# Performance work log

Measured on AMD Instinct MI355X. Metric: run time of the kernel, lower is better.

Reference implementation:

```python
import jax, jax.numpy as jnp
import numpy as np

N, M, D_IN, D_OUT = 100000, 1024, 64, 64


def setup_inputs() -> dict:
    key = jax.random.key(0)
    ks = jax.random.split(key, 8)
    # kaiming_uniform_ bound for fan_in = D_IN: sqrt(6 / fan_in) with a=sqrt(5) default? torch's
    # kaiming_uniform_ default (a=0) gives bound = sqrt(6/fan_in); exact init is irrelevant for math.
    bound = float(np.sqrt(6.0 / D_IN))
    return {
        "x": jax.random.normal(ks[0], (N, D_IN), dtype=jnp.float32),
        "neighbors": jax.random.normal(ks[1], (M, D_IN), dtype=jnp.float32),
        "Wq": jax.random.uniform(ks[2], (D_OUT, D_IN), jnp.float32, -bound, bound),
        "bq": jnp.zeros((D_OUT,), jnp.float32),
        "Wk": jax.random.uniform(ks[3], (D_OUT, D_IN), jnp.float32, -bound, bound),
        "bk": jnp.zeros((D_OUT,), jnp.float32),
        "Wv": jax.random.uniform(ks[4], (D_OUT, D_IN), jnp.float32, -bound, bound),
        "bv": jnp.zeros((D_OUT,), jnp.float32),
    }


def reference(x, neighbors, Wq, bq, Wk, bk, Wv, bv):
    # q: [N, D_OUT], k: [M, D_OUT]
    q = x @ Wq.T + bq
    k = neighbors @ Wk.T + bk
    # scores: [N, M] -- same math as sum(q[:,None,:] * k[None,:,:], axis=2) but via GEMM
    scores = q @ k.T
    attn = jax.nn.softmax(scores, axis=1)
    # attn @ neighbors: [N, D_IN], then value projection -> [N, D_OUT]
    agg = attn @ neighbors
    return agg @ Wv.T + bv
```

## Files before the change

kernel.cpp:

```cpp
#include <hip/hip_runtime.h>


#define N_ROWS 100000

typedef __attribute__((ext_vector_type(8))) _Float16 half8;
typedef __attribute__((ext_vector_type(4))) float    f32x4;

#define MFMA16(a,b,c) __builtin_amdgcn_mfma_f32_16x16x32_f16((a),(b),(c),0,0,0)

static __device__ __forceinline__ f32x4 zero4() {
    f32x4 v = {0.f, 0.f, 0.f, 0.f};
    return v;
}

__global__ __launch_bounds__(256)
void prep_kernel(const float* __restrict__ nb, const float* __restrict__ Wq,
                 const float* __restrict__ bq, const float* __restrict__ Wk,
                 unsigned short* __restrict__ GFh, unsigned short* __restrict__ GFl,
                 float* __restrict__ uW, unsigned short* __restrict__ KF,
                 unsigned short* __restrict__ VF)
{
    __shared__ __align__(16) float sm[8192];
    const int tid = threadIdx.x;
    if (blockIdx.x == 0) {
        const float4* wk4 = (const float4*)Wk;
        const float4* wq4 = (const float4*)Wq;
        float4* dk = (float4*)sm;
        float4* dq = (float4*)(sm + 4096);
        #pragma unroll
        for (int u = 0; u < 4; u++) {
            dk[u * 256 + tid] = wk4[u * 256 + tid];
            dq[u * 256 + tid] = wq4[u * 256 + tid];
        }
        __syncthreads();
        const int e2 = tid & 63, e1g = (tid >> 6) * 16;
        float g[16];
        #pragma unroll
        for (int q = 0; q < 16; q++) g[q] = 0.f;
        for (int w = 0; w < 64; w++) {
            float kv = sm[w * 64 + e2];
            const float* wqp = sm + 4096 + w * 64 + e1g;
            #pragma unroll
            for (int q = 0; q < 16; q++) g[q] = fmaf(wqp[q], kv, g[q]);
        }
        union { half8 h; uint4 u; } ph0, pl0, ph1, pl1;
        #pragma unroll
        for (int i = 0; i < 8; i++) {
            _Float16 h0 = (_Float16)g[i];
            ph0.h[i] = h0; pl0.h[i] = (_Float16)(g[i] - (float)h0);
            _Float16 h1 = (_Float16)g[8 + i];
            ph1.h[i] = h1; pl1.h[i] = (_Float16)(g[8 + i] - (float)h1);
        }
        const int mt = e2 >> 4, cc = e2 & 15;
        const int ks = tid >> 7, Q0 = 2 * ((tid >> 6) & 1);
        const int f  = mt * 2 + ks;
        *(uint4*)(GFh + (f * 64 + Q0 * 16 + cc) * 8)       = ph0.u;
        *(uint4*)(GFh + (f * 64 + (Q0 + 1) * 16 + cc) * 8) = ph1.u;
        *(uint4*)(GFl + (f * 64 + Q0 * 16 + cc) * 8)       = pl0.u;
        *(uint4*)(GFl + (f * 64 + (Q0 + 1) * 16 + cc) * 8) = pl1.u;
        if (tid < 64) {
            float uu = 0.f;
            for (int w = 0; w < 64; w++) uu = fmaf(bq[w], sm[w * 64 + tid], uu);
            uW[tid] = uu;
        }
    } else {
        const int j0 = (blockIdx.x - 1) * 64;
        const int T0 = (blockIdx.x - 1) * 2;
        {
            const int jr = tid >> 2, c0 = (tid & 3) * 16;
            const float* np = nb + (size_t)(j0 + jr) * 64 + c0;
            #pragma unroll
            for (int u = 0; u < 4; u++) {
                float4 v = *(const float4*)(np + 4 * u);
                sm[jr * 65 + c0 + 4 * u]     = v.x;
                sm[jr * 65 + c0 + 4 * u + 1] = v.y;
                sm[jr * 65 + c0 + 4 * u + 2] = v.z;
                sm[jr * 65 + c0 + 4 * u + 3] = v.w;
            }
        }
        #pragma unroll
        for (int s = 0; s < 2; s++) {
            const int slot = tid + 256 * s;
            const int tt = (slot >> 8) & 1, f = (slot >> 6) & 3, ln = slot & 63;
            const int t = f >> 1, h = f & 1, Qw = ln >> 4, cw = ln & 15;
            const int key = ((cw >> 3) & 1) * 16 + ((cw >> 2) & 1) * 8 + 4 * t + (cw & 3);
            const float* kp = nb + (size_t)((T0 + tt) * 32 + key) * 64 + h * 32 + Qw * 8;
            float b[8];
            *(float4*)b       = *(const float4*)kp;
            *(float4*)(b + 4) = *(const float4*)(kp + 4);
            union { half8 hh; uint4 u; } pk;
            #pragma unroll
            for (int i = 0; i < 8; i++) pk.hh[i] = (_Float16)b[i];
            *(uint4*)(KF + (size_t)(T0 + tt) * 2048 + f * 512 + ln * 8) = pk.u;
        }
        __syncthreads();
        #pragma unroll
        for (int s = 0; s < 2; s++) {
            const int slot = tid + 256 * s;
            const int tt = (slot >> 8) & 1, dt = (slot >> 6) & 3, ln = slot & 63;
            const int Qw = ln >> 4, cw = ln & 15;
            union { half8 hh; uint4 u; } pv;
            #pragma unroll
            for (int i = 0; i < 8; i++)
                pv.hh[i] = (_Float16)sm[(tt * 32 + Qw * 8 + i) * 65 + dt * 16 + cw];
            *(uint4*)(VF + (size_t)(T0 + tt) * 2048 + dt * 512 + ln * 8) = pv.u;
        }
    }
}

static __device__ __forceinline__ void flash_step(
    const unsigned short* __restrict__ kfl, const unsigned short* __restrict__ vfl,
    int Tn,
    const half8 (&ck)[4], half8 (&nk)[4], half8 (&vA)[4],
    const half8 (&qh)[2][2], const half8 (&ql)[2][2],
    f32x4 (&acc)[2][4], float (&mrow)[2], float (&lrow)[2])
{
    const unsigned short* kn = kfl + Tn * 2048;
    #pragma unroll
    for (int f = 0; f < 4; f++) nk[f] = *(const half8*)(kn + f * 512);

    f32x4 S[2][2];
    #pragma unroll
    for (int t = 0; t < 2; t++)
        #pragma unroll
        for (int qt = 0; qt < 2; qt++) {
            f32x4 s = MFMA16(ck[2 * t],     qh[qt][0], zero4());
            s = MFMA16(ck[2 * t + 1], qh[qt][1], s);
            s = MFMA16(ck[2 * t],     ql[qt][0], s);
            s = MFMA16(ck[2 * t + 1], ql[qt][1], s);
            S[t][qt] = s;
        }
    half8 pB[2];
    #pragma unroll
    for (int qt = 0; qt < 2; qt++) {
        float pmax = fmaxf(fmaxf(fmaxf(S[0][qt][0], S[0][qt][1]),
                                 fmaxf(S[0][qt][2], S[0][qt][3])),
                           fmaxf(fmaxf(S[1][qt][0], S[1][qt][1]),
                                 fmaxf(S[1][qt][2], S[1][qt][3])));
        if (__any(pmax > mrow[qt] + 8.f)) {
            float cm = pmax;
            cm = fmaxf(cm, __shfl_xor(cm, 16));
            cm = fmaxf(cm, __shfl_xor(cm, 32));
            const float mn = fmaxf(mrow[qt], cm);
            const float sc = __expf(mrow[qt] - mn);
            mrow[qt] = mn;
            lrow[qt] *= sc;
            #pragma unroll
            for (int dt = 0; dt < 4; dt++)
                #pragma unroll
                for (int r = 0; r < 4; r++) acc[qt][dt][r] *= sc;
        }
        const float mref = mrow[qt];
        float p[8]; float ps = 0.f;
        #pragma unroll
        for (int r = 0; r < 4; r++) { p[r] = __expf(S[0][qt][r] - mref); ps += p[r]; }
        #pragma unroll
        for (int r = 0; r < 4; r++) { p[4 + r] = __expf(S[1][qt][r] - mref); ps += p[4 + r]; }
        lrow[qt] += ps;
        #pragma unroll
        for (int i = 0; i < 8; i++) pB[qt][i] = (_Float16)p[i];
    }
    #pragma unroll
    for (int dt = 0; dt < 4; dt++) {
        acc[0][dt] = MFMA16(vA[dt], pB[0], acc[0][dt]);
        acc[1][dt] = MFMA16(vA[dt], pB[1], acc[1][dt]);
    }
    const unsigned short* vn = vfl + Tn * 2048;
    #pragma unroll
    for (int d = 0; d < 4; d++) vA[d] = *(const half8*)(vn + d * 512);
}

__global__ __launch_bounds__(64, 3)
void attn_kernel(const float* __restrict__ x,
                 const unsigned short* __restrict__ GFh,
                 const unsigned short* __restrict__ GFl,
                 const float* __restrict__ uW,
                 const unsigned short* __restrict__ KF,
                 const unsigned short* __restrict__ VF,
                 const float* __restrict__ Wv,
                 const float* __restrict__ bv,
                 float* __restrict__ out)
{
    __shared__ __align__(16) float slice[1088];
    const int lane = threadIdx.x & 63;
    const int Q    = lane >> 4;
    const int c    = lane & 15;
    const int rbase = blockIdx.x * 32;

    half8 qh[2][2], ql[2][2];
    #pragma unroll
    for (int rt = 0; rt < 2; rt++) {
        int row = rbase + rt * 16 + c;
        if (row > N_ROWS - 1) row = N_ROWS - 1;
        half8 xh[2], xl[2];
        #pragma unroll
        for (int ks = 0; ks < 2; ks++) {
            const float* xp = x + (size_t)row * 64 + ks * 32 + Q * 8;
            float a[8];
            *(float4*)a       = *(const float4*)xp;
            *(float4*)(a + 4) = *(const float4*)(xp + 4);
            #pragma unroll
            for (int i = 0; i < 8; i++) {
                _Float16 h = (_Float16)a[i];
                xh[ks][i] = h;
                xl[ks][i] = (_Float16)(a[i] - (float)h);
            }
        }
        #pragma unroll
        for (int mt = 0; mt < 4; mt++) {
            f32x4 Cm = zero4();
            #pragma unroll
            for (int ks = 0; ks < 2; ks++) {
                half8 gh = *(const half8*)(GFh + ((mt * 2 + ks) * 64 + lane) * 8);
                half8 gl = *(const half8*)(GFl + ((mt * 2 + ks) * 64 + lane) * 8);
                Cm = MFMA16(gh, xh[ks], Cm);
                Cm = MFMA16(gh, xl[ks], Cm);
                Cm = MFMA16(gl, xh[ks], Cm);
            }
            *(f32x4*)(slice + c * 68 + mt * 16 + 4 * Q) = Cm;
        }
        __builtin_amdgcn_s_waitcnt(0);
        #pragma unroll
        for (int ks = 0; ks < 2; ks++) {
            const float* qp = slice + c * 68 + ks * 32 + Q * 8;
            const float* up = uW + ks * 32 + Q * 8;
            #pragma unroll
            for (int i = 0; i < 8; i++) {
                float val = qp[i] + up[i];
                _Float16 h = (_Float16)val;
                qh[rt][ks][i] = h;
                ql[rt][ks][i] = (_Float16)(val - (float)h);
            }
        }
        __builtin_amdgcn_s_waitcnt(0);
    }

    f32x4 acc[2][4];
    #pragma unroll
    for (int qt = 0; qt < 2; qt++)
        #pragma unroll
        for (int dt = 0; dt < 4; dt++) acc[qt][dt] = zero4();
    float mrow[2] = { -3.0e38f, -3.0e38f };
    float lrow[2] = { 0.f, 0.f };

    const unsigned short* kfl = KF + lane * 8;
    const unsigned short* vfl = VF + lane * 8;
    half8 kA[4], kB[4], vA[4];
    #pragma unroll
    for (int f = 0; f < 4; f++) kA[f] = *(const half8*)(kfl + f * 512);
    #pragma unroll
    for (int d = 0; d < 4; d++) vA[d] = *(const half8*)(vfl + d * 512);

    #pragma unroll 1
    for (int TT = 0; TT < 16; TT++) {
        flash_step(kfl, vfl, 2 * TT + 1, kA, kB, vA, qh, ql, acc, mrow, lrow);
        const int Tn = (2 * TT + 2 < 32) ? 2 * TT + 2 : 31;
        flash_step(kfl, vfl, Tn,         kB, kA, vA, qh, ql, acc, mrow, lrow);
    }

    #pragma unroll
    for (int qt = 0; qt < 2; qt++) {
        float l = lrow[qt];
        l += __shfl_xor(l, 16);
        l += __shfl_xor(l, 32);
        const float rl = 1.f / l;
        #pragma unroll
        for (int dt = 0; dt < 4; dt++)
            #pragma unroll
            for (int r = 0; r < 4; r++) acc[qt][dt][r] *= rl;
    }
    half8 wf[4][2];
    #pragma unroll
    for (int mt = 0; mt < 4; mt++)
        #pragma unroll
        for (int ks = 0; ks < 2; ks++) {
            const float* wp = Wv + (size_t)(mt * 16 + c) * 64 + ks * 32 + Q * 8;
            #pragma unroll
            for (int i = 0; i < 8; i++) wf[mt][ks][i] = (_Float16)wp[i];
        }
    const int srcA = 32 * (Q & 1) + c;
    const int srcB = srcA + 16;
    const bool hi = (Q >> 1) & 1;
    f32x4 o[2][4];
    #pragma unroll
    for (int qt = 0; qt < 2; qt++) {
        half8 pe[2];
        #pragma unroll
        for (int ks = 0; ks < 2; ks++) {
            #pragma unroll
            for (int r = 0; r < 4; r++) {
                float a0 = __shfl(acc[qt][2 * ks + 0][r], srcA);
                float a1 = __shfl(acc[qt][2 * ks + 1][r], srcA);
                float b0 = __shfl(acc[qt][2 * ks + 0][r], srcB);
                float b1 = __shfl(acc[qt][2 * ks + 1][r], srcB);
                pe[ks][r]     = (_Float16)(hi ? a1 : a0);
                pe[ks][4 + r] = (_Float16)(hi ? b1 : b0);
            }
        }
        #pragma unroll
        for (int mt = 0; mt < 4; mt++) {
            f32x4 t = MFMA16(wf[mt][0], pe[0], zero4());
            o[qt][mt] = MFMA16(wf[mt][1], pe[1], t);
        }
    }
    float4 bf[4];
    #pragma unroll
    for (int mt = 0; mt < 4; mt++) bf[mt] = *(const float4*)(bv + mt * 16 + 4 * Q);
    #pragma unroll
    for (int qt = 0; qt < 2; qt++) {
        const int row = rbase + qt * 16 + c;
        if (row < N_ROWS) {
            #pragma unroll
            for (int mt = 0; mt < 4; mt++) {
                float4 vv = make_float4(o[qt][mt][0] + bf[mt].x, o[qt][mt][1] + bf[mt].y,
                                        o[qt][mt][2] + bf[mt].z, o[qt][mt][3] + bf[mt].w);
                *(float4*)(out + (size_t)row * 64 + mt * 16 + 4 * Q) = vv;
            }
        }
    }
}

extern "C" void kernel_launch(void* const* d_in, const int* in_sizes, int n_in,
                              void* d_out, int out_size, void* d_ws, size_t ws_size,
                              hipStream_t stream)
{
    const float* x  = (const float*)d_in[0];
    const float* nb = (const float*)d_in[1];
    const float* Wq = (const float*)d_in[2];
    const float* bq = (const float*)d_in[3];
    const float* Wk = (const float*)d_in[4];
    const float* Wv = (const float*)d_in[6];
    const float* bv = (const float*)d_in[7];
    float* out = (float*)d_out;

    char* ws = (char*)d_ws;
    unsigned short* GFh = (unsigned short*)(ws);
    unsigned short* GFl = (unsigned short*)(ws + 8192);
    float*          uW  = (float*)(ws + 16384);
    unsigned short* KF  = (unsigned short*)(ws + 16640);
    unsigned short* VF  = (unsigned short*)(ws + 147712);

    prep_kernel<<<17, 256, 0, stream>>>(nb, Wq, bq, Wk, GFh, GFl, uW, KF, VF);
    const int grid = N_ROWS / 32;
    attn_kernel<<<grid, 64, 0, stream>>>(x, GFh, GFl, uW, KF, VF, Wv, bv, out);
}
```

Measured before the change: 149.2 us.

## Split each 32-row block across two waves and use exp2 with prescaled queries

Each block now runs two waves, and each wave handles 16 query rows instead of one wave handling 32. This halves per-wave register state and raises the number of waves available to hide latency. Queries are prescaled by log2(e), so the softmax uses the hardware exp2 directly, and the rescale threshold is adjusted to match. The trade-off is that every wave now loads the full K/V fragments for only 16 rows, which halves K/V reuse per load and doubles L2 traffic for K/V.

```diff
diff --git a/kernel.cpp b/kernel.cpp
--- a/kernel.cpp
+++ b/kernel.cpp
@@ -2,6 +2,7 @@
 
 
 #define N_ROWS 100000
+#define LOG2E 1.44269504088896f
 
 typedef __attribute__((ext_vector_type(8))) _Float16 half8;
 typedef __attribute__((ext_vector_type(4))) float    f32x4;
@@ -112,65 +113,55 @@
     const unsigned short* __restrict__ kfl, const unsigned short* __restrict__ vfl,
     int Tn,
     const half8 (&ck)[4], half8 (&nk)[4], half8 (&vA)[4],
-    const half8 (&qh)[2][2], const half8 (&ql)[2][2],
-    f32x4 (&acc)[2][4], float (&mrow)[2], float (&lrow)[2])
+    const half8 (&qh)[2], const half8 (&ql)[2],
+    f32x4 (&acc)[4], float& mrow, float& lrow)
 {
     const unsigned short* kn = kfl + Tn * 2048;
     #pragma unroll
     for (int f = 0; f < 4; f++) nk[f] = *(const half8*)(kn + f * 512);
 
-    f32x4 S[2][2];
-    #pragma unroll
-    for (int t = 0; t < 2; t++)
-        #pragma unroll
-        for (int qt = 0; qt < 2; qt++) {
-            f32x4 s = MFMA16(ck[2 * t],     qh[qt][0], zero4());
-            s = MFMA16(ck[2 * t + 1], qh[qt][1], s);
-            s = MFMA16(ck[2 * t],     ql[qt][0], s);
-            s = MFMA16(ck[2 * t + 1], ql[qt][1], s);
-            S[t][qt] = s;
-        }
-    half8 pB[2];
-    #pragma unroll
-    for (int qt = 0; qt < 2; qt++) {
-        float pmax = fmaxf(fmaxf(fmaxf(S[0][qt][0], S[0][qt][1]),
-                                 fmaxf(S[0][qt][2], S[0][qt][3])),
-                           fmaxf(fmaxf(S[1][qt][0], S[1][qt][1]),
-                                 fmaxf(S[1][qt][2], S[1][qt][3])));
-        if (__any(pmax > mrow[qt] + 8.f)) {
-            float cm = pmax;
-            cm = fmaxf(cm, __shfl_xor(cm, 16));
-            cm = fmaxf(cm, __shfl_xor(cm, 32));
-            const float mn = fmaxf(mrow[qt], cm);
-            const float sc = __expf(mrow[qt] - mn);
-            mrow[qt] = mn;
-            lrow[qt] *= sc;
-            #pragma unroll
-            for (int dt = 0; dt < 4; dt++)
-                #pragma unroll
-                for (int r = 0; r < 4; r++) acc[qt][dt][r] *= sc;
-        }
-        const float mref = mrow[qt];
-        float p[8]; float ps = 0.f;
-        #pragma unroll
-        for (int r = 0; r < 4; r++) { p[r] = __expf(S[0][qt][r] - mref); ps += p[r]; }
-        #pragma unroll
-        for (int r = 0; r < 4; r++) { p[4 + r] = __expf(S[1][qt][r] - mref); ps += p[4 + r]; }
-        lrow[qt] += ps;
-        #pragma unroll
-        for (int i = 0; i < 8; i++) pB[qt][i] = (_Float16)p[i];
-    }
-    #pragma unroll
-    for (int dt = 0; dt < 4; dt++) {
-        acc[0][dt] = MFMA16(vA[dt], pB[0], acc[0][dt]);
-        acc[1][dt] = MFMA16(vA[dt], pB[1], acc[1][dt]);
-    }
+    f32x4 S[2];
+    #pragma unroll
+    for (int t = 0; t < 2; t++) {
+        f32x4 s = MFMA16(ck[2 * t],     qh[0], zero4());
+        s = MFMA16(ck[2 * t + 1], qh[1], s);
+        s = MFMA16(ck[2 * t],     ql[0], s);
+        s = MFMA16(ck[2 * t + 1], ql[1], s);
+        S[t] = s;
+    }
+    float pmax = fmaxf(fmaxf(fmaxf(S[0][0], S[0][1]), fmaxf(S[0][2], S[0][3])),
+                       fmaxf(fmaxf(S[1][0], S[1][1]), fmaxf(S[1][2], S[1][3])));
+    if (__any(pmax > mrow + 11.5424f)) {
+        float cm = pmax;
+        cm = fmaxf(cm, __shfl_xor(cm, 16));
+        cm = fmaxf(cm, __shfl_xor(cm, 32));
+        const float mn = fmaxf(mrow, cm);
+        const float sc = __builtin_amdgcn_exp2f(mrow - mn);
+        mrow = mn;
+        lrow *= sc;
+        #pragma unroll
+        for (int dt = 0; dt < 4; dt++)
+            #pragma unroll
+            for (int r = 0; r < 4; r++) acc[dt][r] *= sc;
+    }
+    const float mref = mrow;
+    float p[8]; float ps = 0.f;
+    #pragma unroll
+    for (int r = 0; r < 4; r++) { p[r] = __builtin_amdgcn_exp2f(S[0][r] - mref); ps += p[r]; }
+    #pragma unroll
+    for (int r = 0; r < 4; r++) { p[4 + r] = __builtin_amdgcn_exp2f(S[1][r] - mref); ps += p[4 + r]; }
+    lrow += ps;
+    half8 pB;
+    #pragma unroll
+    for (int i = 0; i < 8; i++) pB[i] = (_Float16)p[i];
+    #pragma unroll
+    for (int dt = 0; dt < 4; dt++) acc[dt] = MFMA16(vA[dt], pB, acc[dt]);
     const unsigned short* vn = vfl + Tn * 2048;
     #pragma unroll
     for (int d = 0; d < 4; d++) vA[d] = *(const half8*)(vn + d * 512);
 }
 
-__global__ __launch_bounds__(64, 3)
+__global__ __launch_bounds__(128, 4)
 void attn_kernel(const float* __restrict__ x,
                  const unsigned short* __restrict__ GFh,
                  const unsigned short* __restrict__ GFl,
@@ -181,17 +172,18 @@
                  const float* __restrict__ bv,
                  float* __restrict__ out)
 {
-    __shared__ __align__(16) float slice[1088];
-    const int lane = threadIdx.x & 63;
+    __shared__ __align__(16) float slices[2 * 1088];
+    const int tid  = threadIdx.x;
+    const int lane = tid & 63;
+    const int wv   = tid >> 6;
     const int Q    = lane >> 4;
     const int c    = lane & 15;
-    const int rbase = blockIdx.x * 32;
-
-    half8 qh[2][2], ql[2][2];
-    #pragma unroll
-    for (int rt = 0; rt < 2; rt++) {
-        int row = rbase + rt * 16 + c;
-        if (row > N_ROWS - 1) row = N_ROWS - 1;
+    const int rbase = blockIdx.x * 32 + wv * 16;
+    float* slice = slices + wv * 1088;
+
+    half8 qh[2], ql[2];
+    {
+        const int row = rbase + c;
         half8 xh[2], xl[2];
         #pragma unroll
         for (int ks = 0; ks < 2; ks++) {
@@ -226,22 +218,19 @@
             const float* up = uW + ks * 32 + Q * 8;
             #pragma unroll
             for (int i = 0; i < 8; i++) {
-                float val = qp[i] + up[i];
+                float val = (qp[i] + up[i]) * LOG2E;
                 _Float16 h = (_Float16)val;
-                qh[rt][ks][i] = h;
-                ql[rt][ks][i] = (_Float16)(val - (float)h);
+                qh[ks][i] = h;
+                ql[ks][i] = (_Float16)(val - (float)h);
             }
         }
-        __builtin_amdgcn_s_waitcnt(0);
-    }
-
-    f32x4 acc[2][4];
-    #pragma unroll
-    for (int qt = 0; qt < 2; qt++)
-        #pragma unroll
-        for (int dt = 0; dt < 4; dt++) acc[qt][dt] = zero4();
-    float mrow[2] = { -3.0e38f, -3.0e38f };
-    float lrow[2] = { 0.f, 0.f };
+    }
+
+    f32x4 acc[4];
+    #pragma unroll
+    for (int dt = 0; dt < 4; dt++) acc[dt] = zero4();
+    float mrow = -3.0e38f;
+    float lrow = 0.f;
 
     const unsigned short* kfl = KF + lane * 8;
     const unsigned short* vfl = VF + lane * 8;
@@ -258,16 +247,15 @@
         flash_step(kfl, vfl, Tn,         kB, kA, vA, qh, ql, acc, mrow, lrow);
     }
 
-    #pragma unroll
-    for (int qt = 0; qt < 2; qt++) {
-        float l = lrow[qt];
+    {
+        float l = lrow;
         l += __shfl_xor(l, 16);
         l += __shfl_xor(l, 32);
         const float rl = 1.f / l;
         #pragma unroll
         for (int dt = 0; dt < 4; dt++)
             #pragma unroll
-            for (int r = 0; r < 4; r++) acc[qt][dt][r] *= rl;
+            for (int r = 0; r < 4; r++) acc[dt][r] *= rl;
     }
     half8 wf[4][2];
     #pragma unroll
@@ -281,42 +269,32 @@
     const int srcA = 32 * (Q & 1) + c;
     const int srcB = srcA + 16;
     const bool hi = (Q >> 1) & 1;
-    f32x4 o[2][4];
-    #pragma unroll
-    for (int qt = 0; qt < 2; qt++) {
-        half8 pe[2];
-        #pragma unroll
-        for (int ks = 0; ks < 2; ks++) {
-            #pragma unroll
-            for (int r = 0; r < 4; r++) {
-                float a0 = __shfl(acc[qt][2 * ks + 0][r], srcA);
-                float a1 = __shfl(acc[qt][2 * ks + 1][r], srcA);
-                float b0 = __shfl(acc[qt][2 * ks + 0][r], srcB);
-                float b1 = __shfl(acc[qt][2 * ks + 1][r], srcB);
-                pe[ks][r]     = (_Float16)(hi ? a1 : a0);
-                pe[ks][4 + r] = (_Float16)(hi ? b1 : b0);
-            }
-        }
-        #pragma unroll
-        for (int mt = 0; mt < 4; mt++) {
-            f32x4 t = MFMA16(wf[mt][0], pe[0], zero4());
-            o[qt][mt] = MFMA16(wf[mt][1], pe[1], t);
-        }
-    }
-    float4 bf[4];
-    #pragma unroll
-    for (int mt = 0; mt < 4; mt++) bf[mt] = *(const float4*)(bv + mt * 16 + 4 * Q);
-    #pragma unroll
-    for (int qt = 0; qt < 2; qt++) {
-        const int row = rbase + qt * 16 + c;
-        if (row < N_ROWS) {
-            #pragma unroll
-            for (int mt = 0; mt < 4; mt++) {
-                float4 vv = make_float4(o[qt][mt][0] + bf[mt].x, o[qt][mt][1] + bf[mt].y,
-                                        o[qt][mt][2] + bf[mt].z, o[qt][mt][3] + bf[mt].w);
-                *(float4*)(out + (size_t)row * 64 + mt * 16 + 4 * Q) = vv;
-            }
-        }
+    half8 pe[2];
+    #pragma unroll
+    for (int ks = 0; ks < 2; ks++) {
+        #pragma unroll
+        for (int r = 0; r < 4; r++) {
+            float a0 = __shfl(acc[2 * ks + 0][r], srcA);
+            float a1 = __shfl(acc[2 * ks + 1][r], srcA);
+            float b0 = __shfl(acc[2 * ks + 0][r], srcB);
+            float b1 = __shfl(acc[2 * ks + 1][r], srcB);
+            pe[ks][r]     = (_Float16)(hi ? a1 : a0);
+            pe[ks][4 + r] = (_Float16)(hi ? b1 : b0);
+        }
+    }
+    f32x4 o[4];
+    #pragma unroll
+    for (int mt = 0; mt < 4; mt++) {
+        f32x4 t = MFMA16(wf[mt][0], pe[0], zero4());
+        o[mt] = MFMA16(wf[mt][1], pe[1], t);
+    }
+    const int row = rbase + c;
+    #pragma unroll
+    for (int mt = 0; mt < 4; mt++) {
+        const float4 bf = *(const float4*)(bv + mt * 16 + 4 * Q);
+        float4 vv = make_float4(o[mt][0] + bf.x, o[mt][1] + bf.y,
+                                o[mt][2] + bf.z, o[mt][3] + bf.w);
+        *(float4*)(out + (size_t)row * 64 + mt * 16 + 4 * Q) = vv;
     }
 }
 
@@ -342,5 +320,5 @@
 
     prep_kernel<<<17, 256, 0, stream>>>(nb, Wq, bq, Wk, GFh, GFl, uW, KF, VF);
     const int grid = N_ROWS / 32;
-    attn_kernel<<<grid, 64, 0, stream>>>(x, GFh, GFl, uW, KF, VF, Wv, bv, out);
-}
+    attn_kernel<<<grid, 128, 0, stream>>>(x, GFh, GFl, uW, KF, VF, Wv, bv, out);
+}
```

New measurement: 161.1 us. +8.0%, slower.

## Process two key tiles per flash iteration with base-2 softmax and a shared max gate

Applied to the files above, without the earlier changes.

Restructures the online-softmax loop so each iteration computes scores for two key tiles, runs one rescale check for both, and double-buffers both K and V tiles in registers. Q is pre-scaled by log2(e) so the exponentials use the native exp2 instruction. The rescale gate is adjusted to the base-2 scale so it keeps the same margin. Row bounds checks are dropped, which relies on N being a multiple of 32. Launch bounds move from 3 to 2 waves per SIMD to give the larger register footprint room, at the cost of lower occupancy.

```diff
diff --git a/kernel.cpp b/kernel.cpp
--- a/kernel.cpp
+++ b/kernel.cpp
@@ -2,6 +2,8 @@
 
 
 #define N_ROWS 100000
+#define LOG2E 1.44269504088896f
+#define GATE_THR 11.5424f
 
 typedef __attribute__((ext_vector_type(8))) _Float16 half8;
 typedef __attribute__((ext_vector_type(4))) float    f32x4;
@@ -108,69 +110,7 @@
     }
 }
 
-static __device__ __forceinline__ void flash_step(
-    const unsigned short* __restrict__ kfl, const unsigned short* __restrict__ vfl,
-    int Tn,
-    const half8 (&ck)[4], half8 (&nk)[4], half8 (&vA)[4],
-    const half8 (&qh)[2][2], const half8 (&ql)[2][2],
-    f32x4 (&acc)[2][4], float (&mrow)[2], float (&lrow)[2])
-{
-    const unsigned short* kn = kfl + Tn * 2048;
-    #pragma unroll
-    for (int f = 0; f < 4; f++) nk[f] = *(const half8*)(kn + f * 512);
-
-    f32x4 S[2][2];
-    #pragma unroll
-    for (int t = 0; t < 2; t++)
-        #pragma unroll
-        for (int qt = 0; qt < 2; qt++) {
-            f32x4 s = MFMA16(ck[2 * t],     qh[qt][0], zero4());
-            s = MFMA16(ck[2 * t + 1], qh[qt][1], s);
-            s = MFMA16(ck[2 * t],     ql[qt][0], s);
-            s = MFMA16(ck[2 * t + 1], ql[qt][1], s);
-            S[t][qt] = s;
-        }
-    half8 pB[2];
-    #pragma unroll
-    for (int qt = 0; qt < 2; qt++) {
-        float pmax = fmaxf(fmaxf(fmaxf(S[0][qt][0], S[0][qt][1]),
-                                 fmaxf(S[0][qt][2], S[0][qt][3])),
-                           fmaxf(fmaxf(S[1][qt][0], S[1][qt][1]),
-                                 fmaxf(S[1][qt][2], S[1][qt][3])));
-        if (__any(pmax > mrow[qt] + 8.f)) {
-            float cm = pmax;
-            cm = fmaxf(cm, __shfl_xor(cm, 16));
-            cm = fmaxf(cm, __shfl_xor(cm, 32));
-            const float mn = fmaxf(mrow[qt], cm);
-            const float sc = __expf(mrow[qt] - mn);
-            mrow[qt] = mn;
-            lrow[qt] *= sc;
-            #pragma unroll
-            for (int dt = 0; dt < 4; dt++)
-                #pragma unroll
-                for (int r = 0; r < 4; r++) acc[qt][dt][r] *= sc;
-        }
-        const float mref = mrow[qt];
-        float p[8]; float ps = 0.f;
-        #pragma unroll
-        for (int r = 0; r < 4; r++) { p[r] = __expf(S[0][qt][r] - mref); ps += p[r]; }
-        #pragma unroll
-        for (int r = 0; r < 4; r++) { p[4 + r] = __expf(S[1][qt][r] - mref); ps += p[4 + r]; }
-        lrow[qt] += ps;
-        #pragma unroll
-        for (int i = 0; i < 8; i++) pB[qt][i] = (_Float16)p[i];
-    }
-    #pragma unroll
-    for (int dt = 0; dt < 4; dt++) {
-        acc[0][dt] = MFMA16(vA[dt], pB[0], acc[0][dt]);
-        acc[1][dt] = MFMA16(vA[dt], pB[1], acc[1][dt]);
-    }
-    const unsigned short* vn = vfl + Tn * 2048;
-    #pragma unroll
-    for (int d = 0; d < 4; d++) vA[d] = *(const half8*)(vn + d * 512);
-}
-
-__global__ __launch_bounds__(64, 3)
+__global__ __launch_bounds__(64, 2)
 void attn_kernel(const float* __restrict__ x,
                  const unsigned short* __restrict__ GFh,
                  const unsigned short* __restrict__ GFl,
@@ -190,8 +130,7 @@
     half8 qh[2][2], ql[2][2];
     #pragma unroll
     for (int rt = 0; rt < 2; rt++) {
-        int row = rbase + rt * 16 + c;
-        if (row > N_ROWS - 1) row = N_ROWS - 1;
+        const int row = rbase + rt * 16 + c;
         half8 xh[2], xl[2];
         #pragma unroll
         for (int ks = 0; ks < 2; ks++) {
@@ -226,7 +165,7 @@
             const float* up = uW + ks * 32 + Q * 8;
             #pragma unroll
             for (int i = 0; i < 8; i++) {
-                float val = qp[i] + up[i];
+                float val = (qp[i] + up[i]) * LOG2E;
                 _Float16 h = (_Float16)val;
                 qh[rt][ks][i] = h;
                 ql[rt][ks][i] = (_Float16)(val - (float)h);
@@ -245,17 +184,105 @@
 
     const unsigned short* kfl = KF + lane * 8;
     const unsigned short* vfl = VF + lane * 8;
-    half8 kA[4], kB[4], vA[4];
-    #pragma unroll
-    for (int f = 0; f < 4; f++) kA[f] = *(const half8*)(kfl + f * 512);
-    #pragma unroll
-    for (int d = 0; d < 4; d++) vA[d] = *(const half8*)(vfl + d * 512);
+    half8 kA[4], kB[4], vA[4], vB[4];
+    #pragma unroll
+    for (int f = 0; f < 4; f++) {
+        kA[f] = *(const half8*)(kfl + f * 512);
+        kB[f] = *(const half8*)(kfl + 2048 + f * 512);
+        vA[f] = *(const half8*)(vfl + f * 512);
+        vB[f] = *(const half8*)(vfl + 2048 + f * 512);
+    }
 
     #pragma unroll 1
     for (int TT = 0; TT < 16; TT++) {
-        flash_step(kfl, vfl, 2 * TT + 1, kA, kB, vA, qh, ql, acc, mrow, lrow);
-        const int Tn = (2 * TT + 2 < 32) ? 2 * TT + 2 : 31;
-        flash_step(kfl, vfl, Tn,         kB, kA, vA, qh, ql, acc, mrow, lrow);
+        const int Tn = (TT < 15) ? (2 * TT + 2) : 30;
+
+        f32x4 Sa[2][2], Sb[2][2];
+        #pragma unroll
+        for (int t = 0; t < 2; t++)
+            #pragma unroll
+            for (int qt = 0; qt < 2; qt++) {
+                f32x4 s = MFMA16(kA[2 * t],     qh[qt][0], zero4());
+                s = MFMA16(kA[2 * t + 1], qh[qt][1], s);
+                s = MFMA16(kA[2 * t],     ql[qt][0], s);
+                s = MFMA16(kA[2 * t + 1], ql[qt][1], s);
+                Sa[t][qt] = s;
+                f32x4 u = MFMA16(kB[2 * t],     qh[qt][0], zero4());
+                u = MFMA16(kB[2 * t + 1], qh[qt][1], u);
+                u = MFMA16(kB[2 * t],     ql[qt][0], u);
+                u = MFMA16(kB[2 * t + 1], ql[qt][1], u);
+                Sb[t][qt] = u;
+            }
+        #pragma unroll
+        for (int f = 0; f < 4; f++) {
+            kA[f] = *(const half8*)(kfl + (size_t)Tn * 2048 + f * 512);
+            kB[f] = *(const half8*)(kfl + (size_t)(Tn + 1) * 2048 + f * 512);
+        }
+
+        float pmax[2];
+        #pragma unroll
+        for (int qt = 0; qt < 2; qt++) {
+            float ma = fmaxf(fmaxf(fmaxf(Sa[0][qt][0], Sa[0][qt][1]),
+                                   fmaxf(Sa[0][qt][2], Sa[0][qt][3])),
+                             fmaxf(fmaxf(Sa[1][qt][0], Sa[1][qt][1]),
+                                   fmaxf(Sa[1][qt][2], Sa[1][qt][3])));
+            float mb = fmaxf(fmaxf(fmaxf(Sb[0][qt][0], Sb[0][qt][1]),
+                                   fmaxf(Sb[0][qt][2], Sb[0][qt][3])),
+                             fmaxf(fmaxf(Sb[1][qt][0], Sb[1][qt][1]),
+                                   fmaxf(Sb[1][qt][2], Sb[1][qt][3])));
+            pmax[qt] = fmaxf(ma, mb);
+        }
+        if (__any((pmax[0] > mrow[0] + GATE_THR) | (pmax[1] > mrow[1] + GATE_THR))) {
+            #pragma unroll
+            for (int qt = 0; qt < 2; qt++) {
+                float cm = pmax[qt];
+                cm = fmaxf(cm, __shfl_xor(cm, 16));
+                cm = fmaxf(cm, __shfl_xor(cm, 32));
+                const float mn = fmaxf(mrow[qt], cm);
+                const float sc = __builtin_amdgcn_exp2f(mrow[qt] - mn);
+                mrow[qt] = mn;
+                lrow[qt] *= sc;
+                #pragma unroll
+                for (int dt = 0; dt < 4; dt++)
+                    #pragma unroll
+                    for (int r = 0; r < 4; r++) acc[qt][dt][r] *= sc;
+            }
+        }
+
+        half8 pBa[2], pBb[2];
+        #pragma unroll
+        for (int qt = 0; qt < 2; qt++) {
+            const float mref = mrow[qt];
+            float ps = 0.f;
+            float pa[8], pb[8];
+            #pragma unroll
+            for (int r = 0; r < 4; r++) {
+                pa[r]     = __builtin_amdgcn_exp2f(Sa[0][qt][r] - mref);
+                pa[4 + r] = __builtin_amdgcn_exp2f(Sa[1][qt][r] - mref);
+                pb[r]     = __builtin_amdgcn_exp2f(Sb[0][qt][r] - mref);
+                pb[4 + r] = __builtin_amdgcn_exp2f(Sb[1][qt][r] - mref);
+            }
+            #pragma unroll
+            for (int i = 0; i < 8; i++) { ps += pa[i]; ps += pb[i]; }
+            lrow[qt] += ps;
+            #pragma unroll
+            for (int i = 0; i < 8; i++) {
+                pBa[qt][i] = (_Float16)pa[i];
+                pBb[qt][i] = (_Float16)pb[i];
+            }
+        }
+        #pragma unroll
+        for (int dt = 0; dt < 4; dt++) {
+            acc[0][dt] = MFMA16(vA[dt], pBa[0], acc[0][dt]);
+            acc[1][dt] = MFMA16(vA[dt], pBa[1], acc[1][dt]);
+            acc[0][dt] = MFMA16(vB[dt], pBb[0], acc[0][dt]);
+            acc[1][dt] = MFMA16(vB[dt], pBb[1], acc[1][dt]);
+        }
+        #pragma unroll
+        for (int d = 0; d < 4; d++) {
+            vA[d] = *(const half8*)(vfl + (size_t)Tn * 2048 + d * 512);
+            vB[d] = *(const half8*)(vfl + (size_t)(Tn + 1) * 2048 + d * 512);
+        }
     }
 
     #pragma unroll
@@ -303,19 +330,15 @@
             o[qt][mt] = MFMA16(wf[mt][1], pe[1], t);
         }
     }
-    float4 bf[4];
-    #pragma unroll
-    for (int mt = 0; mt < 4; mt++) bf[mt] = *(const float4*)(bv + mt * 16 + 4 * Q);
     #pragma unroll
     for (int qt = 0; qt < 2; qt++) {
         const int row = rbase + qt * 16 + c;
-        if (row < N_ROWS) {
-            #pragma unroll
-            for (int mt = 0; mt < 4; mt++) {
-                float4 vv = make_float4(o[qt][mt][0] + bf[mt].x, o[qt][mt][1] + bf[mt].y,
-                                        o[qt][mt][2] + bf[mt].z, o[qt][mt][3] + bf[mt].w);
-                *(float4*)(out + (size_t)row * 64 + mt * 16 + 4 * Q) = vv;
-            }
+        #pragma unroll
+        for (int mt = 0; mt < 4; mt++) {
+            const float4 bf = *(const float4*)(bv + mt * 16 + 4 * Q);
+            float4 vv = make_float4(o[qt][mt][0] + bf.x, o[qt][mt][1] + bf.y,
+                                    o[qt][mt][2] + bf.z, o[qt][mt][3] + bf.w);
+            *(float4*)(out + (size_t)row * 64 + mt * 16 + 4 * Q) = vv;
         }
     }
 }
```

New measurement: 150.0 us. About the same (+0.6%).
